# Kernel tuning notes

Measured on AMD Instinct MI355X. Metric: run time of the kernel, lower is better.

Reference implementation:

```python
import jax, jax.numpy as jnp
import numpy as np

D = 1024
H = 16
DH = D // H  # 64
B, S = 4, 1024


def setup_inputs() -> dict:
    key = jax.random.key(0)
    ks = jax.random.split(key, 7)
    sequences = jax.random.normal(ks[0], (B, S, D), dtype=jnp.float32)
    scale = 1.0 / np.sqrt(DH)
    Wq = jax.random.normal(ks[1], (H, DH, DH), dtype=jnp.float32) * scale
    Wk = jax.random.normal(ks[2], (H, DH, DH), dtype=jnp.float32) * scale
    Wv = jax.random.normal(ks[3], (H, DH, DH), dtype=jnp.float32) * scale
    bq = jax.random.normal(ks[4], (H, DH), dtype=jnp.float32) * 0.01
    bk = jax.random.normal(ks[5], (H, DH), dtype=jnp.float32) * 0.01
    bv = jax.random.normal(ks[6], (H, DH), dtype=jnp.float32) * 0.01
    return {"sequences": sequences, "Wq": Wq, "Wk": Wk, "Wv": Wv,
            "bq": bq, "bk": bk, "bv": bv}


def reference(sequences, Wq, Wk, Wv, bq, bk, bv):
    b, s, d = sequences.shape
    x = sequences.reshape(b, s, H, DH)  # split channels into heads
    # per-head Linear: y = x @ W.T + b (torch convention)
    q = jnp.einsum('bshd,hed->bshe', x, Wq) + bq
    k = jnp.einsum('bshd,hed->bshe', x, Wk) + bk
    v = jnp.einsum('bshd,hed->bshe', x, Wv) + bv
    inv_sqrt_dh = jnp.asarray(1.0 / np.sqrt(DH), dtype=sequences.dtype)
    scores = jnp.einsum('bshe,bthe->bhst', q, k) * inv_sqrt_dh  # [B,H,S,S]
    attn = jax.nn.softmax(scores, axis=-1)
    out = jnp.einsum('bhst,bthe->bshe', attn, v)  # [B,S,H,DH]
    return out.reshape(b, s, d)  # hstack of heads == reshape here
```

## Files before the change

### kernel.cpp

```cpp
#include <hip/hip_runtime.h>

#define H 16
#define DH 64
#define BB 4
#define SS 1024
#define DD 1024

typedef __attribute__((ext_vector_type(8))) short bf16x8;
typedef __attribute__((ext_vector_type(4))) float f32x4;
typedef __attribute__((ext_vector_type(4))) unsigned int u32x4;
typedef _Float16 f16x4 __attribute__((ext_vector_type(4)));
typedef __fp16 hf16x2 __attribute__((ext_vector_type(2)));

#define QSCALE 0.18033688011112042f

__device__ __forceinline__ unsigned short f2bf(float f) {
    union { float f; unsigned u; } v; v.f = f;
    unsigned u = v.u;
    return (unsigned short)((u + 0x7FFFu + ((u >> 16) & 1u)) >> 16);
}

__device__ __forceinline__ unsigned short f2h(float f) {
    union { _Float16 h; unsigned short u; } v;
    v.h = (_Float16)f;
    return v.u;
}

__device__ __forceinline__ void pack8(unsigned short* dst, f32x4 a, f32x4 b) {
    unsigned u0 = (unsigned)f2bf(a[0]) | ((unsigned)f2bf(a[1]) << 16);
    unsigned u1 = (unsigned)f2bf(a[2]) | ((unsigned)f2bf(a[3]) << 16);
    unsigned u2 = (unsigned)f2bf(b[0]) | ((unsigned)f2bf(b[1]) << 16);
    unsigned u3 = (unsigned)f2bf(b[2]) | ((unsigned)f2bf(b[3]) << 16);
    u32x4 v = {u0, u1, u2, u3};
    *(u32x4*)dst = v;
}

__device__ __forceinline__ void async_cp1k(const unsigned short* g,
                                           unsigned short* l, int lane) {
    __builtin_amdgcn_global_load_lds(
        (const __attribute__((address_space(1))) unsigned int*)(g + lane * 8),
        (__attribute__((address_space(3))) unsigned int*)l, 16, 0, 0);
}

__global__ __launch_bounds__(256) void wprep_kernel(
    const float* __restrict__ Wq, const float* __restrict__ Wk,
    const float* __restrict__ Wv, unsigned short* __restrict__ Wp)
{
    const int tg = blockIdx.x * 256 + threadIdx.x;
    const int r = tg >> 2, part = tg & 3;
    const int e = r & 63, hm = r >> 6;
    const int m = hm % 3, h = hm / 3;
    const float* src = (m == 0 ? Wq : (m == 1 ? Wk : Wv)) +
                       (size_t)(h * 64 + e) * 64 + part * 16;
    const float scale = (m == 0) ? QSCALE : 1.0f;
    f32x4 f0 = ((const f32x4*)src)[0];
    f32x4 f1 = ((const f32x4*)src)[1];
    f32x4 f2 = ((const f32x4*)src)[2];
    f32x4 f3 = ((const f32x4*)src)[3];
    f0 *= scale; f1 *= scale; f2 *= scale; f3 *= scale;
    unsigned short tmp[16];
    pack8(tmp, f0, f1);
    pack8(tmp + 8, f2, f3);
    unsigned short* dst = Wp + (size_t)(hm * 64 + e) * 64;
    const int c0 = part * 2, sw = e & 7;
    *(u32x4*)(dst + (c0 ^ sw) * 8)       = *(const u32x4*)tmp;
    *(u32x4*)(dst + ((c0 + 1) ^ sw) * 8) = *(const u32x4*)(tmp + 8);
}

__global__ __launch_bounds__(256) void qkv_kernel(
    const float* __restrict__ x, const unsigned short* __restrict__ Wp,
    const float* __restrict__ bq, const float* __restrict__ bk,
    const float* __restrict__ bv,
    unsigned short* __restrict__ Qg, unsigned short* __restrict__ Kg,
    unsigned short* __restrict__ VTg)
{
    __shared__ __align__(16) unsigned short Xl[4096];
    __shared__ __align__(16) unsigned short Wl[12288];

    const int bid = blockIdx.x;
    const int sc = bid & 15, h = (bid >> 4) & 15, b = bid >> 8;
    const int s0 = sc * 64;
    const int tid = threadIdx.x;
    const int lane = tid & 63, w = tid >> 6;

    {
        const unsigned short* wbase = Wp + (size_t)h * 12288;
#pragma unroll
        for (int sub = 0; sub < 6; sub++) {
            const int off = w * 3072 + sub * 512;
            async_cp1k(wbase + off, &Wl[off], lane);
        }
    }
    {
        const int s = tid >> 2, part = tid & 3;
        const float* src = x + ((size_t)(b * SS + s0 + s)) * DD + h * DH + part * 16;
        f32x4 f0 = ((const f32x4*)src)[0];
        f32x4 f1 = ((const f32x4*)src)[1];
        f32x4 f2 = ((const f32x4*)src)[2];
        f32x4 f3 = ((const f32x4*)src)[3];
        unsigned short tmp[16];
        pack8(tmp, f0, f1);
        pack8(tmp + 8, f2, f3);
        const int c0 = part * 2, sws = s & 7;
        *(u32x4*)&Xl[s * 64 + (c0 ^ sws) * 8]       = *(const u32x4*)tmp;
        *(u32x4*)&Xl[s * 64 + ((c0 + 1) ^ sws) * 8] = *(const u32x4*)(tmp + 8);
    }
    __syncthreads();

    const int l15 = lane & 15, quad = lane >> 4, sw = l15 & 7;

    f32x4 acc[3][4];
#pragma unroll
    for (int m = 0; m < 3; m++)
#pragma unroll
        for (int nt = 0; nt < 4; nt++) acc[m][nt] = (f32x4){0.f, 0.f, 0.f, 0.f};

#pragma unroll
    for (int k2 = 0; k2 < 2; k2++) {
        const int csw = (((k2 << 2) | quad) ^ sw) * 8;
        bf16x8 a = *(const bf16x8*)&Xl[(w * 16 + l15) * 64 + csw];
#pragma unroll
        for (int nt = 0; nt < 4; nt++) {
            const int boff = (nt * 16 + l15) * 64 + csw;
            bf16x8 b0 = *(const bf16x8*)&Wl[boff];
            acc[0][nt] = __builtin_amdgcn_mfma_f32_16x16x32_bf16(a, b0, acc[0][nt], 0, 0, 0);
            bf16x8 b1 = *(const bf16x8*)&Wl[4096 + boff];
            acc[1][nt] = __builtin_amdgcn_mfma_f32_16x16x32_bf16(a, b1, acc[1][nt], 0, 0, 0);
            bf16x8 b2 = *(const bf16x8*)&Wl[8192 + boff];
            acc[2][nt] = __builtin_amdgcn_mfma_f32_16x16x32_bf16(a, b2, acc[2][nt], 0, 0, 0);
        }
    }
    __syncthreads();

#pragma unroll
    for (int nt = 0; nt < 4; nt++) {
        const int e = nt * 16 + l15;
        const float bqs = bq[h * DH + e] * QSCALE;
        const float bks = bk[h * DH + e];
        const float bvs = bv[h * DH + e];
#pragma unroll
        for (int r = 0; r < 4; r++) {
            const int srow = w * 16 + quad * 4 + r;
            Xl[srow * 64 + e]        = f2bf(acc[0][nt][r] + bqs);
            Wl[srow * 64 + e]        = f2bf(acc[1][nt][r] + bks);
            Wl[4096 + e * 64 + srow] = f2h(acc[2][nt][r] + bvs);
        }
    }
    __syncthreads();
    {
        const size_t bh = (size_t)(b * H + h);
        const int row = tid >> 2, part = tid & 3;
        const int cg = part * 16, c0 = part * 2, swr = row & 7;
        unsigned short* qdst = Qg + (bh * SS + s0 + row) * DH + cg;
        *(u32x4*)qdst       = *(const u32x4*)&Xl[row * 64 + cg];
        *(u32x4*)(qdst + 8) = *(const u32x4*)&Xl[row * 64 + cg + 8];
        unsigned short* kbase = Kg + (bh * 16 + sc) * 4096 + row * 64;
        *(u32x4*)(kbase + (c0 ^ swr) * 8)       = *(const u32x4*)&Wl[row * 64 + c0 * 8];
        *(u32x4*)(kbase + ((c0 + 1) ^ swr) * 8) = *(const u32x4*)&Wl[row * 64 + c0 * 8 + 8];
        unsigned short* vbase = VTg + (bh * 16 + sc) * 4096 + row * 64;
        *(u32x4*)(vbase + (c0 ^ swr) * 8)       = *(const u32x4*)&Wl[4096 + row * 64 + c0 * 8];
        *(u32x4*)(vbase + ((c0 + 1) ^ swr) * 8) = *(const u32x4*)&Wl[4096 + row * 64 + c0 * 8 + 8];
    }
}

__global__ __launch_bounds__(256) void attn_kernel(
    const unsigned short* __restrict__ Qg, const unsigned short* __restrict__ Kg,
    const unsigned short* __restrict__ VTg, float* __restrict__ out)
{
    __shared__ __align__(16) unsigned short Kl[2][4096];
    __shared__ __align__(16) unsigned short Vl[2][4096];

    const int bid = blockIdx.x;
    const int bh = bid & 63, qg = bid >> 6;
    const int h = bh & 15, b = bh >> 4;
    const int tid = threadIdx.x;
    const int lane = tid & 63, w = tid >> 6;
    const int l15 = lane & 15, quad = lane >> 4, sw = l15 & 7;

    const unsigned short* Kt = Kg + (size_t)bh * 16 * 4096;
    const unsigned short* Vt = VTg + (size_t)bh * 16 * 4096;

    bf16x8 aQ[2][2];
#pragma unroll
    for (int j = 0; j < 2; j++) {
        const int qrow = (qg * 2 + j) * 64 + w * 16 + l15;
        const unsigned short* qp = Qg + ((size_t)bh * SS + qrow) * DH + quad * 8;
        aQ[j][0] = *(const bf16x8*)(qp);
        aQ[j][1] = *(const bf16x8*)(qp + 32);
    }

    {
        const int off = w * 1024;
        async_cp1k(Kt + off,       &Kl[0][off],       lane);
        async_cp1k(Kt + off + 512, &Kl[0][off + 512], lane);
        async_cp1k(Vt + off,       &Vl[0][off],       lane);
        async_cp1k(Vt + off + 512, &Vl[0][off + 512], lane);
    }

    f32x4 accO[2][4];
#pragma unroll
    for (int j = 0; j < 2; j++)
#pragma unroll
        for (int et = 0; et < 4; et++) accO[j][et] = (f32x4){0.f, 0.f, 0.f, 0.f};
    float rs_acc[2] = {0.f, 0.f};

    for (int kt = 0; kt < 16; kt++) {
        __syncthreads();
        const unsigned short* Kc = Kl[kt & 1];
        const unsigned short* Vc = Vl[kt & 1];
        if (kt < 15) {
            const unsigned short* kg = Kt + (kt + 1) * 4096;
            const unsigned short* vg = Vt + (kt + 1) * 4096;
            unsigned short* Kn = Kl[(kt + 1) & 1];
            unsigned short* Vn = Vl[(kt + 1) & 1];
            const int off = w * 1024;
            async_cp1k(kg + off,       Kn + off,       lane);
            async_cp1k(kg + off + 512, Kn + off + 512, lane);
            async_cp1k(vg + off,       Vn + off,       lane);
            async_cp1k(vg + off + 512, Vn + off + 512, lane);
        }

        bf16x8 aK[4][2];
        f16x4 aV[4][4];
#pragma unroll
        for (int nt = 0; nt < 4; nt++) {
#pragma unroll
            for (int k2 = 0; k2 < 2; k2++)
                aK[nt][k2] = *(const bf16x8*)
                    &Kc[(nt * 16 + l15) * 64 + ((((k2 << 2) | quad)) ^ sw) * 8];
        }
#pragma unroll
        for (int et = 0; et < 4; et++) {
#pragma unroll
            for (int nt = 0; nt < 4; nt++) {
                const int c = 2 * nt + (quad >> 1);
                aV[et][nt] = *(const f16x4*)
                    &Vc[(et * 16 + l15) * 64 + (c ^ sw) * 8 + (quad & 1) * 4];
            }
        }

#pragma unroll
        for (int j = 0; j < 2; j++) {
            f32x4 sc[4];
#pragma unroll
            for (int nt = 0; nt < 4; nt++) {
                f32x4 z = {0.f, 0.f, 0.f, 0.f};
                z = __builtin_amdgcn_mfma_f32_16x16x32_bf16(aK[nt][0], aQ[j][0], z, 0, 0, 0);
                z = __builtin_amdgcn_mfma_f32_16x16x32_bf16(aK[nt][1], aQ[j][1], z, 0, 0, 0);
                sc[nt] = z;
            }

            float rs = 0.f;
            f16x4 pf[4];
#pragma unroll
            for (int nt = 0; nt < 4; nt++) {
                float p0 = exp2f(sc[nt][0]);
                float p1 = exp2f(sc[nt][1]);
                float p2 = exp2f(sc[nt][2]);
                float p3 = exp2f(sc[nt][3]);
                rs += (p0 + p1) + (p2 + p3);
                union { hf16x2 h; unsigned u; } lo, hi;
                lo.h = __builtin_amdgcn_cvt_pkrtz(p0, p1);
                hi.h = __builtin_amdgcn_cvt_pkrtz(p2, p3);
                union { unsigned u[2]; f16x4 v; } pk;
                pk.u[0] = lo.u; pk.u[1] = hi.u;
                pf[nt] = pk.v;
            }
            rs_acc[j] += rs;

#pragma unroll
            for (int et = 0; et < 4; et++) {
#pragma unroll
                for (int nt = 0; nt < 4; nt++)
                    accO[j][et] = __builtin_amdgcn_mfma_f32_16x16x16f16(
                        aV[et][nt], pf[nt], accO[j][et], 0, 0, 0);
            }
        }
    }

#pragma unroll
    for (int j = 0; j < 2; j++) {
        float rs = rs_acc[j];
        rs += __shfl_xor(rs, 16);
        rs += __shfl_xor(rs, 32);
        const float inv = 1.0f / rs;
        const int srow = (qg * 2 + j) * 64 + w * 16 + l15;
        float* op = out + ((size_t)b * SS + srow) * DD + h * DH;
#pragma unroll
        for (int et = 0; et < 4; et++) {
            f32x4 v = accO[j][et] * inv;
            *(f32x4*)(op + et * 16 + quad * 4) = v;
        }
    }
}

extern "C" void kernel_launch(void* const* d_in, const int* in_sizes, int n_in,
                              void* d_out, int out_size, void* d_ws, size_t ws_size,
                              hipStream_t stream) {
    const float* x  = (const float*)d_in[0];
    const float* Wq = (const float*)d_in[1];
    const float* Wk = (const float*)d_in[2];
    const float* Wv = (const float*)d_in[3];
    const float* bq = (const float*)d_in[4];
    const float* bk = (const float*)d_in[5];
    const float* bv = (const float*)d_in[6];

    const size_t NE = (size_t)BB * H * SS * DH;
    unsigned short* Qg  = (unsigned short*)d_ws;
    unsigned short* Kg  = Qg + NE;
    unsigned short* VTg = Kg + NE;
    unsigned short* Wp  = VTg + NE;

    wprep_kernel<<<48, 256, 0, stream>>>(Wq, Wk, Wv, Wp);
    qkv_kernel<<<BB * H * (SS / 64), 256, 0, stream>>>(x, Wp, bq, bk, bv,
                                                       Qg, Kg, VTg);
    attn_kernel<<<BB * H * 8, 256, 0, stream>>>(Qg, Kg, VTg, (float*)d_out);
}
```

Before: 125.7 us.

## Load K/V fragments directly from global memory instead of LDS double-buffering

The attention kernel drops its LDS double-buffered async copies of K and V tiles and the per-iteration barrier, reading MFMA operands straight from global memory (L2/cache) in plain row-major layout. The projection kernel writes K and V without the XOR swizzle that only served LDS bank-conflict avoidance. The score MFMAs for both query groups are issued before the softmax, and the loop is unrolled by two to expose more independent work. This removes the barrier and LDS traffic, but each wave now fetches K/V separately from global memory with higher latency and no explicit prefetch.

```diff
diff --git a/kernel.cpp b/kernel.cpp
--- a/kernel.cpp
+++ b/kernel.cpp
@@ -149,17 +149,16 @@
     __syncthreads();
     {
         const size_t bh = (size_t)(b * H + h);
-        const int row = tid >> 2, part = tid & 3;
-        const int cg = part * 16, c0 = part * 2, swr = row & 7;
+        const int row = tid >> 2, cg = (tid & 3) * 16;
         unsigned short* qdst = Qg + (bh * SS + s0 + row) * DH + cg;
         *(u32x4*)qdst       = *(const u32x4*)&Xl[row * 64 + cg];
         *(u32x4*)(qdst + 8) = *(const u32x4*)&Xl[row * 64 + cg + 8];
-        unsigned short* kbase = Kg + (bh * 16 + sc) * 4096 + row * 64;
-        *(u32x4*)(kbase + (c0 ^ swr) * 8)       = *(const u32x4*)&Wl[row * 64 + c0 * 8];
-        *(u32x4*)(kbase + ((c0 + 1) ^ swr) * 8) = *(const u32x4*)&Wl[row * 64 + c0 * 8 + 8];
-        unsigned short* vbase = VTg + (bh * 16 + sc) * 4096 + row * 64;
-        *(u32x4*)(vbase + (c0 ^ swr) * 8)       = *(const u32x4*)&Wl[4096 + row * 64 + c0 * 8];
-        *(u32x4*)(vbase + ((c0 + 1) ^ swr) * 8) = *(const u32x4*)&Wl[4096 + row * 64 + c0 * 8 + 8];
+        unsigned short* kdst = Kg + (bh * SS + s0 + row) * DH + cg;
+        *(u32x4*)kdst       = *(const u32x4*)&Wl[row * 64 + cg];
+        *(u32x4*)(kdst + 8) = *(const u32x4*)&Wl[row * 64 + cg + 8];
+        unsigned short* vdst = VTg + (bh * 16 + sc) * 4096 + row * 64 + cg;
+        *(u32x4*)vdst       = *(const u32x4*)&Wl[4096 + row * 64 + cg];
+        *(u32x4*)(vdst + 8) = *(const u32x4*)&Wl[4096 + row * 64 + cg + 8];
     }
 }
 
@@ -167,17 +166,14 @@
     const unsigned short* __restrict__ Qg, const unsigned short* __restrict__ Kg,
     const unsigned short* __restrict__ VTg, float* __restrict__ out)
 {
-    __shared__ __align__(16) unsigned short Kl[2][4096];
-    __shared__ __align__(16) unsigned short Vl[2][4096];
-
     const int bid = blockIdx.x;
     const int bh = bid & 63, qg = bid >> 6;
     const int h = bh & 15, b = bh >> 4;
     const int tid = threadIdx.x;
     const int lane = tid & 63, w = tid >> 6;
-    const int l15 = lane & 15, quad = lane >> 4, sw = l15 & 7;
-
-    const unsigned short* Kt = Kg + (size_t)bh * 16 * 4096;
+    const int l15 = lane & 15, quad = lane >> 4;
+
+    const unsigned short* Kt = Kg + (size_t)bh * SS * DH;
     const unsigned short* Vt = VTg + (size_t)bh * 16 * 4096;
 
     bf16x8 aQ[2][2];
@@ -189,14 +185,6 @@
         aQ[j][1] = *(const bf16x8*)(qp + 32);
     }
 
-    {
-        const int off = w * 1024;
-        async_cp1k(Kt + off,       &Kl[0][off],       lane);
-        async_cp1k(Kt + off + 512, &Kl[0][off + 512], lane);
-        async_cp1k(Vt + off,       &Vl[0][off],       lane);
-        async_cp1k(Vt + off + 512, &Vl[0][off + 512], lane);
-    }
-
     f32x4 accO[2][4];
 #pragma unroll
     for (int j = 0; j < 2; j++)
@@ -204,60 +192,47 @@
         for (int et = 0; et < 4; et++) accO[j][et] = (f32x4){0.f, 0.f, 0.f, 0.f};
     float rs_acc[2] = {0.f, 0.f};
 
+#pragma unroll 2
     for (int kt = 0; kt < 16; kt++) {
-        __syncthreads();
-        const unsigned short* Kc = Kl[kt & 1];
-        const unsigned short* Vc = Vl[kt & 1];
-        if (kt < 15) {
-            const unsigned short* kg = Kt + (kt + 1) * 4096;
-            const unsigned short* vg = Vt + (kt + 1) * 4096;
-            unsigned short* Kn = Kl[(kt + 1) & 1];
-            unsigned short* Vn = Vl[(kt + 1) & 1];
-            const int off = w * 1024;
-            async_cp1k(kg + off,       Kn + off,       lane);
-            async_cp1k(kg + off + 512, Kn + off + 512, lane);
-            async_cp1k(vg + off,       Vn + off,       lane);
-            async_cp1k(vg + off + 512, Vn + off + 512, lane);
-        }
+        const unsigned short* kp = Kt + kt * 4096;
+        const unsigned short* vp = Vt + kt * 4096;
 
         bf16x8 aK[4][2];
-        f16x4 aV[4][4];
-#pragma unroll
-        for (int nt = 0; nt < 4; nt++) {
+#pragma unroll
+        for (int nt = 0; nt < 4; nt++)
 #pragma unroll
             for (int k2 = 0; k2 < 2; k2++)
                 aK[nt][k2] = *(const bf16x8*)
-                    &Kc[(nt * 16 + l15) * 64 + ((((k2 << 2) | quad)) ^ sw) * 8];
-        }
-#pragma unroll
-        for (int et = 0; et < 4; et++) {
-#pragma unroll
-            for (int nt = 0; nt < 4; nt++) {
-                const int c = 2 * nt + (quad >> 1);
+                    &kp[(nt * 16 + l15) * 64 + k2 * 32 + quad * 8];
+        f16x4 aV[4][4];
+#pragma unroll
+        for (int et = 0; et < 4; et++)
+#pragma unroll
+            for (int nt = 0; nt < 4; nt++)
                 aV[et][nt] = *(const f16x4*)
-                    &Vc[(et * 16 + l15) * 64 + (c ^ sw) * 8 + (quad & 1) * 4];
-            }
-        }
-
-#pragma unroll
-        for (int j = 0; j < 2; j++) {
-            f32x4 sc[4];
+                    &vp[(et * 16 + l15) * 64 + nt * 16 + quad * 4];
+
+        f32x4 sc[2][4];
+#pragma unroll
+        for (int j = 0; j < 2; j++)
 #pragma unroll
             for (int nt = 0; nt < 4; nt++) {
                 f32x4 z = {0.f, 0.f, 0.f, 0.f};
                 z = __builtin_amdgcn_mfma_f32_16x16x32_bf16(aK[nt][0], aQ[j][0], z, 0, 0, 0);
                 z = __builtin_amdgcn_mfma_f32_16x16x32_bf16(aK[nt][1], aQ[j][1], z, 0, 0, 0);
-                sc[nt] = z;
+                sc[j][nt] = z;
             }
 
+#pragma unroll
+        for (int j = 0; j < 2; j++) {
             float rs = 0.f;
             f16x4 pf[4];
 #pragma unroll
             for (int nt = 0; nt < 4; nt++) {
-                float p0 = exp2f(sc[nt][0]);
-                float p1 = exp2f(sc[nt][1]);
-                float p2 = exp2f(sc[nt][2]);
-                float p3 = exp2f(sc[nt][3]);
+                float p0 = exp2f(sc[j][nt][0]);
+                float p1 = exp2f(sc[j][nt][1]);
+                float p2 = exp2f(sc[j][nt][2]);
+                float p3 = exp2f(sc[j][nt][3]);
                 rs += (p0 + p1) + (p2 + p3);
                 union { hf16x2 h; unsigned u; } lo, hi;
                 lo.h = __builtin_amdgcn_cvt_pkrtz(p0, p1);
@@ -269,12 +244,11 @@
             rs_acc[j] += rs;
 
 #pragma unroll
-            for (int et = 0; et < 4; et++) {
+            for (int et = 0; et < 4; et++)
 #pragma unroll
                 for (int nt = 0; nt < 4; nt++)
                     accO[j][et] = __builtin_amdgcn_mfma_f32_16x16x16f16(
                         aV[et][nt], pf[nt], accO[j][et], 0, 0, 0);
-            }
         }
     }
 
```

After: 178.6 us. 1.42x slower.

## Permute V^T key order for 16-byte LDS reads and unroll double-buffer loop

Applied to the files above, without the earlier changes.

Changes how the projection kernel writes V^T so that key indices within each 64-key tile are permuted (quad*16 + w*4 + r). The attention kernel can then fetch V fragments with two 16-byte LDS reads per output tile instead of four 8-byte reads. The permutation lines up with the per-lane order of the P fragment, so the sum over keys is unchanged. The double-buffer loop is unrolled by two with separate static LDS arrays and precomputed swizzled offsets, which removes the runtime buffer index arithmetic. All QK score MFMAs are now issued before the exp stage, which may raise register pressure.

```diff
diff --git a/kernel.cpp b/kernel.cpp
--- a/kernel.cpp
+++ b/kernel.cpp
@@ -10,6 +10,7 @@
 typedef __attribute__((ext_vector_type(4))) float f32x4;
 typedef __attribute__((ext_vector_type(4))) unsigned int u32x4;
 typedef _Float16 f16x4 __attribute__((ext_vector_type(4)));
+typedef _Float16 f16x8 __attribute__((ext_vector_type(8)));
 typedef __fp16 hf16x2 __attribute__((ext_vector_type(2)));
 
 #define QSCALE 0.18033688011112042f
@@ -141,9 +142,9 @@
 #pragma unroll
         for (int r = 0; r < 4; r++) {
             const int srow = w * 16 + quad * 4 + r;
-            Xl[srow * 64 + e]        = f2bf(acc[0][nt][r] + bqs);
-            Wl[srow * 64 + e]        = f2bf(acc[1][nt][r] + bks);
-            Wl[4096 + e * 64 + srow] = f2h(acc[2][nt][r] + bvs);
+            Xl[srow * 64 + e] = f2bf(acc[0][nt][r] + bqs);
+            Wl[srow * 64 + e] = f2bf(acc[1][nt][r] + bks);
+            Wl[4096 + e * 64 + quad * 16 + w * 4 + r] = f2h(acc[2][nt][r] + bvs);
         }
     }
     __syncthreads();
@@ -167,8 +168,8 @@
     const unsigned short* __restrict__ Qg, const unsigned short* __restrict__ Kg,
     const unsigned short* __restrict__ VTg, float* __restrict__ out)
 {
-    __shared__ __align__(16) unsigned short Kl[2][4096];
-    __shared__ __align__(16) unsigned short Vl[2][4096];
+    __shared__ __align__(16) unsigned short Kl0[4096], Kl1[4096];
+    __shared__ __align__(16) unsigned short Vl0[4096], Vl1[4096];
 
     const int bid = blockIdx.x;
     const int bh = bid & 63, qg = bid >> 6;
@@ -180,6 +181,11 @@
     const unsigned short* Kt = Kg + (size_t)bh * 16 * 4096;
     const unsigned short* Vt = VTg + (size_t)bh * 16 * 4096;
 
+    const int kb0 = l15 * 64 + ((quad)     ^ sw) * 8;
+    const int kb1 = l15 * 64 + ((4 | quad) ^ sw) * 8;
+    const int vb0 = l15 * 64 + (((quad << 1))     ^ sw) * 8;
+    const int vb1 = l15 * 64 + (((quad << 1) | 1) ^ sw) * 8;
+
     bf16x8 aQ[2][2];
 #pragma unroll
     for (int j = 0; j < 2; j++) {
@@ -191,10 +197,10 @@
 
     {
         const int off = w * 1024;
-        async_cp1k(Kt + off,       &Kl[0][off],       lane);
-        async_cp1k(Kt + off + 512, &Kl[0][off + 512], lane);
-        async_cp1k(Vt + off,       &Vl[0][off],       lane);
-        async_cp1k(Vt + off + 512, &Vl[0][off + 512], lane);
+        async_cp1k(Kt + off,       Kl0 + off,       lane);
+        async_cp1k(Kt + off + 512, Kl0 + off + 512, lane);
+        async_cp1k(Vt + off,       Vl0 + off,       lane);
+        async_cp1k(Vt + off + 512, Vl0 + off + 512, lane);
     }
 
     f32x4 accO[2][4];
@@ -204,15 +210,12 @@
         for (int et = 0; et < 4; et++) accO[j][et] = (f32x4){0.f, 0.f, 0.f, 0.f};
     float rs_acc[2] = {0.f, 0.f};
 
-    for (int kt = 0; kt < 16; kt++) {
+    auto step = [&](int kt, const unsigned short* Kc, const unsigned short* Vc,
+                    unsigned short* Kn, unsigned short* Vn) {
         __syncthreads();
-        const unsigned short* Kc = Kl[kt & 1];
-        const unsigned short* Vc = Vl[kt & 1];
         if (kt < 15) {
             const unsigned short* kg = Kt + (kt + 1) * 4096;
             const unsigned short* vg = Vt + (kt + 1) * 4096;
-            unsigned short* Kn = Kl[(kt + 1) & 1];
-            unsigned short* Vn = Vl[(kt + 1) & 1];
             const int off = w * 1024;
             async_cp1k(kg + off,       Kn + off,       lane);
             async_cp1k(kg + off + 512, Kn + off + 512, lane);
@@ -221,43 +224,39 @@
         }
 
         bf16x8 aK[4][2];
-        f16x4 aV[4][4];
 #pragma unroll
         for (int nt = 0; nt < 4; nt++) {
-#pragma unroll
-            for (int k2 = 0; k2 < 2; k2++)
-                aK[nt][k2] = *(const bf16x8*)
-                    &Kc[(nt * 16 + l15) * 64 + ((((k2 << 2) | quad)) ^ sw) * 8];
-        }
+            aK[nt][0] = *(const bf16x8*)(Kc + kb0 + nt * 1024);
+            aK[nt][1] = *(const bf16x8*)(Kc + kb1 + nt * 1024);
+        }
+        f16x8 aV01[4], aV23[4];
 #pragma unroll
         for (int et = 0; et < 4; et++) {
-#pragma unroll
-            for (int nt = 0; nt < 4; nt++) {
-                const int c = 2 * nt + (quad >> 1);
-                aV[et][nt] = *(const f16x4*)
-                    &Vc[(et * 16 + l15) * 64 + (c ^ sw) * 8 + (quad & 1) * 4];
-            }
-        }
-
-#pragma unroll
-        for (int j = 0; j < 2; j++) {
-            f32x4 sc[4];
+            aV01[et] = *(const f16x8*)(Vc + vb0 + et * 1024);
+            aV23[et] = *(const f16x8*)(Vc + vb1 + et * 1024);
+        }
+
+        f32x4 sc[2][4];
+#pragma unroll
+        for (int j = 0; j < 2; j++)
 #pragma unroll
             for (int nt = 0; nt < 4; nt++) {
                 f32x4 z = {0.f, 0.f, 0.f, 0.f};
                 z = __builtin_amdgcn_mfma_f32_16x16x32_bf16(aK[nt][0], aQ[j][0], z, 0, 0, 0);
                 z = __builtin_amdgcn_mfma_f32_16x16x32_bf16(aK[nt][1], aQ[j][1], z, 0, 0, 0);
-                sc[nt] = z;
+                sc[j][nt] = z;
             }
 
+#pragma unroll
+        for (int j = 0; j < 2; j++) {
             float rs = 0.f;
             f16x4 pf[4];
 #pragma unroll
             for (int nt = 0; nt < 4; nt++) {
-                float p0 = exp2f(sc[nt][0]);
-                float p1 = exp2f(sc[nt][1]);
-                float p2 = exp2f(sc[nt][2]);
-                float p3 = exp2f(sc[nt][3]);
+                float p0 = exp2f(sc[j][nt][0]);
+                float p1 = exp2f(sc[j][nt][1]);
+                float p2 = exp2f(sc[j][nt][2]);
+                float p3 = exp2f(sc[j][nt][3]);
                 rs += (p0 + p1) + (p2 + p3);
                 union { hf16x2 h; unsigned u; } lo, hi;
                 lo.h = __builtin_amdgcn_cvt_pkrtz(p0, p1);
@@ -270,12 +269,21 @@
 
 #pragma unroll
             for (int et = 0; et < 4; et++) {
-#pragma unroll
-                for (int nt = 0; nt < 4; nt++)
-                    accO[j][et] = __builtin_amdgcn_mfma_f32_16x16x16f16(
-                        aV[et][nt], pf[nt], accO[j][et], 0, 0, 0);
+                f16x4 v0 = __builtin_shufflevector(aV01[et], aV01[et], 0, 1, 2, 3);
+                f16x4 v1 = __builtin_shufflevector(aV01[et], aV01[et], 4, 5, 6, 7);
+                f16x4 v2 = __builtin_shufflevector(aV23[et], aV23[et], 0, 1, 2, 3);
+                f16x4 v3 = __builtin_shufflevector(aV23[et], aV23[et], 4, 5, 6, 7);
+                accO[j][et] = __builtin_amdgcn_mfma_f32_16x16x16f16(v0, pf[0], accO[j][et], 0, 0, 0);
+                accO[j][et] = __builtin_amdgcn_mfma_f32_16x16x16f16(v1, pf[1], accO[j][et], 0, 0, 0);
+                accO[j][et] = __builtin_amdgcn_mfma_f32_16x16x16f16(v2, pf[2], accO[j][et], 0, 0, 0);
+                accO[j][et] = __builtin_amdgcn_mfma_f32_16x16x16f16(v3, pf[3], accO[j][et], 0, 0, 0);
             }
         }
+    };
+
+    for (int i = 0; i < 8; i++) {
+        step(2 * i,     Kl0, Vl0, Kl1, Vl1);
+        step(2 * i + 1, Kl1, Vl1, Kl0, Vl0);
     }
 
 #pragma unroll
```

Result: faster. 120.6 us (-4.1%).
